# Optimization experiments

Measured on AMD Instinct MI355X. Metric: run time of the kernel, lower is better.

## Reference

```python
import math
import jax, jax.numpy as jnp
import numpy as np

B, C, NH, H, W = 8, 512, 4, 64, 64
CH = C // 8          # qkv channels = 64
HC = CH // NH        # head channels = 16


def _pos_encoding(c, h, w):
    # Faithful to torch code, including the raw memory reinterpretation of
    # pos_h (h, c) -> (1, c, h, 1) and pos_w (c//2, 2w) -> (1, c, 1, w).
    ph = jnp.arange(h, dtype=jnp.float32)[:, None]            # (h, 1)
    pw = jnp.arange(w, dtype=jnp.float32)[None, :]            # (1, w)
    div = jnp.exp(jnp.arange(0, c, 2, dtype=jnp.float32) * (-(math.log(10000.0) / c)))
    pos_h = ph * div[None, :]                                  # (h, c/2)
    pos_w = pw * div[:, None]                                  # (c/2, w)
    pos_h = jnp.concatenate([jnp.sin(pos_h), jnp.cos(pos_h)], axis=1)  # (h, c)
    pos_w = jnp.concatenate([jnp.sin(pos_w), jnp.cos(pos_w)], axis=1)  # (c/2, 2w)
    pos_h = pos_h.reshape(1, c, h, 1)   # raw view, as in torch
    pos_w = pos_w.reshape(1, c, 1, w)   # raw view, as in torch
    return pos_h + pos_w                # (1, c, h, w)


def _conv1x1(x, w, b):
    return jnp.einsum('bchw,oc->bohw', x, w) + b[None, :, None, None]


def setup_inputs() -> dict:
    key = jax.random.key(0)
    ks = jax.random.split(key, 6)
    s = 0.02
    return {
        'x':  jax.random.normal(ks[0], (B, C, H, W), dtype=jnp.float32),
        'wq': jax.random.normal(ks[1], (CH, C), dtype=jnp.float32) * s,
        'bq': jnp.zeros((CH,), dtype=jnp.float32),
        'wk': jax.random.normal(ks[2], (CH, C), dtype=jnp.float32) * s,
        'bk': jnp.zeros((CH,), dtype=jnp.float32),
        'wv': jax.random.normal(ks[3], (CH, C), dtype=jnp.float32) * s,
        'bv': jnp.zeros((CH,), dtype=jnp.float32),
        'wo': jax.random.normal(ks[4], (C, CH), dtype=jnp.float32) * s,
        'bo': jnp.zeros((C,), dtype=jnp.float32),
        'gamma': jnp.full((1,), 0.5, dtype=jnp.float32),  # nonzero to exercise whole graph
    }


def reference(x, wq, bq, wk, bk, wv, bv, wo, bo, gamma):
    b, c, h, w = x.shape
    nh, hc = NH, HC
    x = x + _pos_encoding(c, h, w)

    q = _conv1x1(x, wq, bq).reshape(b, nh, hc, h, w)
    k = _conv1x1(x, wk, bk).reshape(b, nh, hc, h, w)
    v = _conv1x1(x, wv, bv).reshape(b, nh, hc, h, w)

    # column (H) and row (W) views
    q_H = q.transpose(0, 1, 4, 2, 3).reshape(b * nh * w, hc, h).transpose(0, 2, 1)  # (bnw, h, hc)
    q_W = q.transpose(0, 1, 3, 2, 4).reshape(b * nh * h, hc, w).transpose(0, 2, 1)  # (bnh, w, hc)
    k_H = k.transpose(0, 1, 4, 2, 3).reshape(b * nh * w, hc, h)
    k_W = k.transpose(0, 1, 3, 2, 4).reshape(b * nh * h, hc, w)
    v_H = v.transpose(0, 1, 4, 2, 3).reshape(b * nh * w, hc, h)
    v_W = v.transpose(0, 1, 3, 2, 4).reshape(b * nh * h, hc, w)

    inf_mask = jnp.where(jnp.eye(h, dtype=bool), -jnp.inf, 0.0).astype(x.dtype)  # (h, h)
    energy_H = (jnp.matmul(q_H, k_H) + inf_mask[None]).reshape(b, nh, w, h, h).transpose(0, 2, 1, 3, 4)  # (b,w,nh,h,h)
    energy_W = jnp.matmul(q_W, k_W).reshape(b, nh, h, w, w).transpose(0, 2, 1, 3, 4)                     # (b,h,nh,w,w)

    conc = jax.nn.softmax(jnp.concatenate([energy_H, energy_W], axis=4), axis=4)  # (b,w,nh,h,h+w)

    att_H = conc[..., :h].transpose(0, 2, 1, 3, 4).reshape(b * nh * w, h, h)
    # NOTE: faithful to torch: (b,h,nh,w,w) is flattened in (b,h,nh) order
    att_W = conc[..., h:h + w].reshape(b * nh * h, w, w)

    out_H = jnp.matmul(v_H, att_H.transpose(0, 2, 1))
    out_H = out_H.reshape(b, nh, w, hc, h).transpose(0, 3, 4, 1, 2).reshape(b, nh * hc, h, w)
    out_W = jnp.matmul(v_W, att_W.transpose(0, 2, 1))
    out_W = out_W.reshape(b, nh, h, hc, w).transpose(0, 3, 1, 4, 2).reshape(b, nh * hc, h, w)

    out = _conv1x1(out_H + out_W, wo, bo)
    return gamma * out + x
```

## Files before the change

kernel.cpp:

```cpp
#include <hip/hip_runtime.h>
#include <math.h>


typedef unsigned int u32;
typedef unsigned short u16;
typedef __attribute__((ext_vector_type(8))) short short8;
typedef __attribute__((ext_vector_type(4))) float f32x4;

__device__ __forceinline__ u16 f2bf(float v) {
    u32 u = __float_as_uint(v);
    u32 r = (u + 0x7FFFu + ((u >> 16) & 1u)) >> 16;
    return (u16)r;
}

__device__ __forceinline__ float bf2f(u16 v) {
    return __uint_as_float(((u32)v) << 16);
}

__device__ __forceinline__ void gll16(const void* g, void* l) {
    __builtin_amdgcn_global_load_lds(
        (const __attribute__((address_space(1))) u32*)g,
        (__attribute__((address_space(3))) u32*)l, 16, 0, 0);
}

__global__ __launch_bounds__(64) void pos_kernel(float* __restrict__ PH,
                                                 float* __restrict__ PW) {
    const float r = 0.03597789207798663f;
    int c = blockIdx.x;
    int t = threadIdx.x;
    int i = c >> 3;
    int j = ((c & 7) << 6) | t;
    float ph;
    if (j < 256) ph = sinf((float)i * expf(-(float)j * r));
    else         ph = cosf((float)i * expf(-(float)(j - 256) * r));
    PH[c * 64 + t] = ph;
    int tt = c >> 1;
    float dv = expf(-(float)tt * r);
    PW[c * 64 + t] = (c & 1) ? cosf((float)t * dv) : sinf((float)t * dv);
}

__global__ __launch_bounds__(256) void wconv_kernel(
    const float* __restrict__ wq, const float* __restrict__ wk,
    const float* __restrict__ wv, const float* __restrict__ wo,
    u16* __restrict__ WT, u16* __restrict__ WOb) {
    int i = blockIdx.x * 256 + threadIdx.x;
    if (i < 98304) {
        float v;
        if (i < 32768)      v = wq[i];
        else if (i < 65536) v = wk[i - 32768];
        else                v = wv[i - 65536];
        WT[i] = f2bf(v);
    } else {
        WOb[i - 98304] = f2bf(wo[i - 98304]);
    }
}

__global__ __launch_bounds__(256) void wpos_kernel(
    const float* __restrict__ wq, const float* __restrict__ wk,
    const float* __restrict__ wv,
    const float* __restrict__ PH, const float* __restrict__ PW,
    float* __restrict__ WPH3, float* __restrict__ WPW3) {
    int gid = blockIdx.x * 256 + threadIdx.x;
    int h = gid & 63;
    int m = (gid >> 6) & 63;
    int t = gid >> 12;
    int mg = t >> 1, tbl = t & 1;
    const float* W = (mg == 0) ? wq : (mg == 1) ? wk : wv;
    const float* P = tbl ? PW : PH;
    const float* wr = W + m * 512;
    float s = 0.f;
#pragma unroll 8
    for (int c = 0; c < 512; ++c) s += wr[c] * P[c * 64 + h];
    (tbl ? WPW3 : WPH3)[(mg * 64 + m) * 64 + h] = s;
}

__global__ __launch_bounds__(256) void qkvx_kernel(
    const float* __restrict__ x, const u16* __restrict__ WT,
    const float* __restrict__ bq, const float* __restrict__ bk,
    const float* __restrict__ bv,
    const float* __restrict__ WPH3, const float* __restrict__ WPW3,
    u16* __restrict__ QHt, u16* __restrict__ QWt,
    u16* __restrict__ KHt, u16* __restrict__ KWt,
    u16* __restrict__ VHt, u16* __restrict__ Vb) {
    __shared__ u16 Wb[192 * 64];
    __shared__ u16 Bb[64 * 64];
    int L  = blockIdx.x;
    int b  = L & 7;
    int pt = L >> 3;
    int tid  = threadIdx.x;
    int w    = tid >> 6;
    int lane = tid & 63;
    int ln15 = lane & 15, quad = lane >> 4;

    f32x4 acc[12];
#pragma unroll
    for (int mf = 0; mf < 12; ++mf) acc[mf] = (f32x4){0.f, 0.f, 0.f, 0.f};

    const float* xb = x + (size_t)b * 2097152 + pt * 64;

    for (int kc = 0; kc < 512; kc += 64) {
        __syncthreads();
#pragma unroll
        for (int it = 0; it < 6; ++it) {
            int idx = tid + it * 256;
            int r = idx >> 3, s = idx & 7;
            gll16(WT + r * 512 + kc + ((s ^ (r & 7)) * 8), &Wb[idx * 8]);
        }
#pragma unroll
        for (int j = 0; j < 2; ++j) {
            int cc = w + j * 4;
            const float* xp = xb + (size_t)(kc + cc * 8) * 4096 + lane;
            float v[8];
#pragma unroll
            for (int i = 0; i < 8; ++i) v[i] = xp[(size_t)i * 4096];
            short8 pk;
#pragma unroll
            for (int i = 0; i < 8; ++i) pk[i] = (short)f2bf(v[i]);
            *(short8*)&Bb[lane * 64 + ((cc ^ (lane & 7)) * 8)] = pk;
        }
        __syncthreads();
#pragma unroll
        for (int ks = 0; ks < 2; ++ks) {
            int cs = ks * 4 + quad;
            int brow = w * 16 + ln15;
            short8 bf = *(const short8*)&Bb[brow * 64 + ((cs ^ (brow & 7)) * 8)];
#pragma unroll
            for (int mf = 0; mf < 12; ++mf) {
                int arow = mf * 16 + ln15;
                short8 af = *(const short8*)&Wb[arow * 64 + ((cs ^ (arow & 7)) * 8)];
                acc[mf] = __builtin_amdgcn_mfma_f32_16x16x32_bf16(
                    af, bf, acc[mf], 0, 0, 0);
            }
        }
    }

    int wc = w * 16 + ln15;
#pragma unroll
    for (int mf = 0; mf < 12; ++mf) {
        int mg = mf >> 2, nm = mf & 3;
        const float* bias = (mg == 0) ? bq : (mg == 1) ? bk : bv;
        float vals[4];
#pragma unroll
        for (int reg = 0; reg < 4; ++reg) {
            int m2 = nm * 16 + quad * 4 + reg;
            vals[reg] = acc[mf][reg] + bias[m2]
                      + WPH3[(mg * 64 + m2) * 64 + pt]
                      + WPW3[(mg * 64 + m2) * 64 + wc];
        }
        if (mg == 2) {
#pragma unroll
            for (int reg = 0; reg < 4; ++reg) {
                int hc = quad * 4 + reg;
                u16 bv16 = f2bf(vals[reg]);
                VHt[(((b * 4 + nm) * 64 + wc) * 16 + hc) * 64 + pt] = bv16;
                Vb[((size_t)(b * 64 + nm * 16 + hc)) * 4096 + pt * 64 + wc] = bv16;
            }
        } else {
            u16* Ht = (mg == 1) ? KHt : QHt;
            u16* Wt = (mg == 1) ? KWt : QWt;
            ushort4 pk;
            pk.x = f2bf(vals[0]);
            pk.y = f2bf(vals[1]);
            pk.z = f2bf(vals[2]);
            pk.w = f2bf(vals[3]);
            *(ushort4*)&Ht[(((b * 4 + nm) * 64 + wc) * 64 + pt) * 16 + quad * 4] = pk;
            *(ushort4*)&Wt[(((b * 4 + nm) * 64 + pt) * 64 + wc) * 16 + quad * 4] = pk;
        }
    }
}

__global__ __launch_bounds__(256, 4) void attn_kernel(
    const u16* __restrict__ QHt, const u16* __restrict__ QWt,
    const u16* __restrict__ KHt, const u16* __restrict__ KWt,
    const u16* __restrict__ VHt, const u16* __restrict__ Vb,
    u16* __restrict__ OHc, u16* __restrict__ OWc) {
    __shared__ u16 U[11008];
    u16* A_lds  = U;
    u16* B_lds  = U + 2560;
    u16* P_lds  = U;
    u16* VH_lds = U + 8704;
    u16* VW_lds = U + 9856;

    int a = blockIdx.x, n = blockIdx.y, b = blockIdx.z;
    int tid  = threadIdx.x;
    int w    = tid >> 6;
    int lane = tid & 63;
    int ln15 = lane & 15, quad = lane >> 4;
    int nv = a >> 4;
    int hv = ((a & 15) << 2) | n;

    const int cb = ((b * 4 + n) * 64 + a) << 10;
    const u16* vb = Vb + ((size_t)(b * 64 + nv * 16)) * 4096 + hv * 64;

    {
        int t = tid & 127;
        const short8 z8 = {0, 0, 0, 0, 0, 0, 0, 0};
        if (tid < 128) {
            short8 vA = *(const short8*)(QHt + cb + t * 8);
            *(short8*)&A_lds[(t >> 1) * 40 + (t & 1) * 8] = vA;
            short8 vK = *(const short8*)(KHt + cb + t * 8);
            *(short8*)&B_lds[(t >> 1) * 48 + (t & 1) * 8] = vK;
            *(short8*)&B_lds[(t >> 1) * 48 + 16 + (t & 1) * 8] = z8;
            short8 vV = *(const short8*)(VHt + cb + t * 8);
            *(short8*)&VH_lds[(t >> 3) * 72 + (t & 7) * 8] = vV;
        } else {
            short8 vA = *(const short8*)(QWt + cb + t * 8);
            *(short8*)&A_lds[(t >> 1) * 40 + 16 + (t & 1) * 8] = vA;
            short8 vK = *(const short8*)(KWt + cb + t * 8);
            *(short8*)&B_lds[(64 + (t >> 1)) * 48 + 16 + (t & 1) * 8] = vK;
            *(short8*)&B_lds[(64 + (t >> 1)) * 48 + (t & 1) * 8] = z8;
            short8 vV = *(const short8*)(vb + (t >> 3) * 4096 + (t & 7) * 8);
            *(short8*)&VW_lds[(t >> 3) * 72 + (t & 7) * 8] = vV;
        }
    }
    __syncthreads();

    const f32x4 zf = {0.f, 0.f, 0.f, 0.f};
    short8 af = *(const short8*)&A_lds[(w * 16 + ln15) * 40 + quad * 8];
    f32x4 acc[8];
#pragma unroll
    for (int nt = 0; nt < 8; ++nt) {
        short8 bf = *(const short8*)&B_lds[(nt * 16 + ln15) * 48 + quad * 8];
        acc[nt] = __builtin_amdgcn_mfma_f32_16x16x32_bf16(af, bf, zf, 0, 0, 0);
    }

#pragma unroll
    for (int nt = 0; nt < 4; ++nt)
#pragma unroll
        for (int r = 0; r < 4; ++r)
            if (nt * 16 + ln15 == w * 16 + quad * 4 + r) acc[nt][r] = -1e30f;

    float inv[4];
#pragma unroll
    for (int r = 0; r < 4; ++r) {
        float mrow = acc[0][r];
#pragma unroll
        for (int nt = 1; nt < 8; ++nt) mrow = fmaxf(mrow, acc[nt][r]);
        mrow = fmaxf(mrow, __shfl_xor(mrow, 1, 64));
        mrow = fmaxf(mrow, __shfl_xor(mrow, 2, 64));
        mrow = fmaxf(mrow, __shfl_xor(mrow, 4, 64));
        mrow = fmaxf(mrow, __shfl_xor(mrow, 8, 64));
        float s = 0.f;
#pragma unroll
        for (int nt = 0; nt < 8; ++nt) {
            float e = __expf(acc[nt][r] - mrow);
            acc[nt][r] = e;
            s += e;
        }
        s += __shfl_xor(s, 1, 64);
        s += __shfl_xor(s, 2, 64);
        s += __shfl_xor(s, 4, 64);
        s += __shfl_xor(s, 8, 64);
        inv[r] = 1.0f / s;
    }
    __syncthreads();
#pragma unroll
    for (int nt = 0; nt < 8; ++nt)
#pragma unroll
        for (int r = 0; r < 4; ++r)
            P_lds[(w * 16 + quad * 4 + r) * 136 + nt * 16 + ln15] =
                f2bf(acc[nt][r] * inv[r]);
    __syncthreads();

    int prow = (w * 16 + ln15) * 136;
    short8 a0 = *(const short8*)&P_lds[prow +       quad * 8];
    short8 a1 = *(const short8*)&P_lds[prow + 32  + quad * 8];
    short8 a2 = *(const short8*)&P_lds[prow + 64  + quad * 8];
    short8 a3 = *(const short8*)&P_lds[prow + 96  + quad * 8];
    short8 b0 = *(const short8*)&VH_lds[ln15 * 72 +      quad * 8];
    short8 b1 = *(const short8*)&VH_lds[ln15 * 72 + 32 + quad * 8];
    short8 c0 = *(const short8*)&VW_lds[ln15 * 72 +      quad * 8];
    short8 c1 = *(const short8*)&VW_lds[ln15 * 72 + 32 + quad * 8];
    f32x4 oH = __builtin_amdgcn_mfma_f32_16x16x32_bf16(a0, b0, zf, 0, 0, 0);
    oH = __builtin_amdgcn_mfma_f32_16x16x32_bf16(a1, b1, oH, 0, 0, 0);
    f32x4 oW = __builtin_amdgcn_mfma_f32_16x16x32_bf16(a2, c0, zf, 0, 0, 0);
    oW = __builtin_amdgcn_mfma_f32_16x16x32_bf16(a3, c1, oW, 0, 0, 0);

    __syncthreads();
    u16* eph = U;
    u16* epw = U + 16 * 68;
#pragma unroll
    for (int r = 0; r < 4; ++r) {
        eph[(quad * 4 + r) * 68 + ln15 * 4 + w]   = f2bf(oH[r]);
        epw[(w * 16 + quad * 4 + r) * 20 + ln15]  = f2bf(oW[r]);
    }
    __syncthreads();
    {
        int t = tid;
        ushort4 vh = *(const ushort4*)&eph[(t >> 4) * 68 + (t & 15) * 4];
        ushort4 vw = *(const ushort4*)&epw[(t >> 2) * 20 + (t & 3) * 4];
        size_t cbase = (((size_t)b * 4 + n) * 64 + a) * 1024;
        *(ushort4*)&OHc[cbase + t * 4] = vh;
        *(ushort4*)&OWc[cbase + t * 4] = vw;
    }
}

__global__ __launch_bounds__(256) void sconv_kernel(
    const u16* __restrict__ OHc, const u16* __restrict__ OWc,
    u16* __restrict__ Sb) {
    int h = blockIdx.x;
    int b = blockIdx.y;
    int t  = threadIdx.x;
    int wp = t >> 2;
    int cq = t & 3;

    const u16* ohp = OHc + ((((size_t)b * 4 + (h & 3)) * 64 + wp) * 1024
                            + (h >> 2) * 64 + cq * 16);
    short8 oh0 = *(const short8*)ohp;
    short8 oh1 = *(const short8*)(ohp + 8);

    const u16* owb = OWc + (((size_t)b * 4 + (wp & 3)) * 64) * 1024 + h * 16 + cq * 4;
    ushort4 owv[4];
#pragma unroll
    for (int nvi = 0; nvi < 4; ++nvi)
        owv[nvi] = *(const ushort4*)(owb + (size_t)((nvi << 4) | (wp >> 2)) * 1024);

    u16 res[16];
#pragma unroll
    for (int j = 0; j < 16; ++j) {
        u16 ohv = (j < 8) ? (u16)oh0[j] : (u16)oh1[j - 8];
        const ushort4& q = owv[j & 3];
        u16 owu = (j >> 2) == 0 ? q.x : (j >> 2) == 1 ? q.y : (j >> 2) == 2 ? q.z : q.w;
        res[j] = f2bf(bf2f(ohv) + bf2f(owu));
    }
    u16* dst = Sb + (((size_t)b * 4096 + h * 64 + wp) * 64 + cq * 16);
    *(short8*)dst       = *(short8*)&res[0];
    *(short8*)(dst + 8) = *(short8*)&res[8];
}

__global__ __launch_bounds__(256, 4) void finalm_kernel(
    const u16* __restrict__ Sb, const u16* __restrict__ WOb,
    const float* __restrict__ bo, const float* __restrict__ gamma,
    const float* __restrict__ x, const float* __restrict__ PH,
    const float* __restrict__ PW, float* __restrict__ out) {
    __shared__ u16 Ab[64 * 64];
    __shared__ u16 Bb[128 * 64];
    int pt = blockIdx.x;
    int mc = blockIdx.y;
    int b  = blockIdx.z;
    int tid  = threadIdx.x;
    int w    = tid >> 6;
    int lane = tid & 63;
    int ln15 = lane & 15, quad = lane >> 4;
    int p0 = pt * 128, m0 = mc * 64;

    float4 xv[4][2];
#pragma unroll
    for (int mf = 0; mf < 4; ++mf) {
        int m = m0 + mf * 16 + ln15;
#pragma unroll
        for (int pf = 0; pf < 2; ++pf) {
            int pb = p0 + w * 32 + pf * 16 + quad * 4;
            xv[mf][pf] = *(const float4*)&x[((size_t)(b * 512 + m)) * 4096 + pb];
        }
    }

    const u16* Ag = WOb + m0 * 64;
    const u16* Sg = Sb + ((size_t)b * 4096 + p0) * 64;

#pragma unroll
    for (int it = 0; it < 2; ++it) {
        int idx = tid + it * 256;
        int r = idx >> 3, s = idx & 7;
        gll16(Ag + r * 64 + ((s ^ (r & 7)) * 8), &Ab[idx * 8]);
    }
#pragma unroll
    for (int it = 0; it < 4; ++it) {
        int idx = tid + it * 256;
        int r = idx >> 3, s = idx & 7;
        gll16(Sg + r * 64 + ((s ^ (r & 7)) * 8), &Bb[idx * 8]);
    }
    __syncthreads();

    const f32x4 zf = {0.f, 0.f, 0.f, 0.f};
    f32x4 acc[4][2];
#pragma unroll
    for (int mf = 0; mf < 4; ++mf)
#pragma unroll
        for (int pf = 0; pf < 2; ++pf)
            acc[mf][pf] = zf;
#pragma unroll
    for (int ks = 0; ks < 2; ++ks) {
        int cs = ks * 4 + quad;
        short8 af[2], bf[4];
#pragma unroll
        for (int pf = 0; pf < 2; ++pf) {
            int row = w * 32 + pf * 16 + ln15;
            af[pf] = *(const short8*)&Bb[row * 64 + ((cs ^ (row & 7)) * 8)];
        }
#pragma unroll
        for (int mf = 0; mf < 4; ++mf) {
            int row = mf * 16 + ln15;
            bf[mf] = *(const short8*)&Ab[row * 64 + ((cs ^ (row & 7)) * 8)];
        }
#pragma unroll
        for (int mf = 0; mf < 4; ++mf)
#pragma unroll
            for (int pf = 0; pf < 2; ++pf)
                acc[mf][pf] = __builtin_amdgcn_mfma_f32_16x16x32_bf16(
                    af[pf], bf[mf], acc[mf][pf], 0, 0, 0);
    }

    float g = gamma[0];
    int h = pt * 2 + (w >> 1);
    int plb = (w & 1) * 32;
#pragma unroll
    for (int mf = 0; mf < 4; ++mf) {
        int m = m0 + mf * 16 + ln15;
        float bm = bo[m];
        float ph = PH[m * 64 + h];
#pragma unroll
        for (int pf = 0; pf < 2; ++pf) {
            int pb = p0 + w * 32 + pf * 16 + quad * 4;
            size_t o = ((size_t)(b * 512 + m)) * 4096 + pb;
            float4 pwv = *(const float4*)&PW[m * 64 + plb + pf * 16 + quad * 4];
            float4 res;
            res.x = g * (acc[mf][pf][0] + bm) + xv[mf][pf].x + ph + pwv.x;
            res.y = g * (acc[mf][pf][1] + bm) + xv[mf][pf].y + ph + pwv.y;
            res.z = g * (acc[mf][pf][2] + bm) + xv[mf][pf].z + ph + pwv.z;
            res.w = g * (acc[mf][pf][3] + bm) + xv[mf][pf].w + ph + pwv.w;
            *(float4*)&out[o] = res;
        }
    }
}

extern "C" void kernel_launch(void* const* d_in, const int* in_sizes, int n_in,
                              void* d_out, int out_size, void* d_ws, size_t ws_size,
                              hipStream_t stream) {
    const float* x     = (const float*)d_in[0];
    const float* wq    = (const float*)d_in[1];
    const float* bq    = (const float*)d_in[2];
    const float* wk    = (const float*)d_in[3];
    const float* bk    = (const float*)d_in[4];
    const float* wv    = (const float*)d_in[5];
    const float* bv    = (const float*)d_in[6];
    const float* wo    = (const float*)d_in[7];
    const float* bo    = (const float*)d_in[8];
    const float* gamma = (const float*)d_in[9];
    float* out = (float*)d_out;
    float* ws  = (float*)d_ws;

    float* PH   = ws;
    float* PW   = PH + 32768;
    float* WPH3 = PW + 32768;
    float* WPW3 = WPH3 + 12288;
    u16*   WT   = (u16*)(WPW3 + 12288);
    u16*   WOb  = WT + 98304;
    u16*   QHt  = WOb + 32768;
    u16*   QWt  = QHt + 2097152;
    u16*   KHt  = QWt + 2097152;
    u16*   KWt  = KHt + 2097152;
    u16*   VHt  = KWt + 2097152;
    u16*   Vb   = VHt + 2097152;
    u16*   OHc  = Vb  + 2097152;
    u16*   OWc  = OHc + 2097152;
    u16*   Sbb  = OWc + 2097152;

    pos_kernel<<<dim3(512), dim3(64), 0, stream>>>(PH, PW);
    wconv_kernel<<<dim3(512), dim3(256), 0, stream>>>(wq, wk, wv, wo, WT, WOb);
    wpos_kernel<<<dim3(96), dim3(256), 0, stream>>>(wq, wk, wv, PH, PW, WPH3, WPW3);
    qkvx_kernel<<<dim3(512), dim3(256), 0, stream>>>(
        x, WT, bq, bk, bv, WPH3, WPW3, QHt, QWt, KHt, KWt, VHt, Vb);
    attn_kernel<<<dim3(64, 4, 8), dim3(256), 0, stream>>>(
        QHt, QWt, KHt, KWt, VHt, Vb, OHc, OWc);
    sconv_kernel<<<dim3(64, 8), dim3(256), 0, stream>>>(OHc, OWc, Sbb);
    finalm_kernel<<<dim3(32, 8, 8), dim3(256), 0, stream>>>(
        Sbb, WOb, bo, gamma, x, PH, PW, out);
}
```

Measured before the change: 207.3 us.

## Double-buffer QKV projection LDS tiles and retile warps as 2x2 MFMA grid

The QKV projection kernel now double-buffers its weight and x tiles in LDS. The next K-chunk's global loads are issued before the MFMAs on the current chunk, and the bf16 conversion and store happen after them, so memory latency overlaps with compute and there is one barrier per step instead of two. Warps are also remapped from 12 M-fragments by 1 N-fragment to 6 by 2, which lowers the LDS A-fragment reads per MFMA. The cost is double the LDS footprint (about 57KB) and extra registers for the prefetched x values, which may reduce occupancy.

```diff
diff --git a/kernel.cpp b/kernel.cpp
--- a/kernel.cpp
+++ b/kernel.cpp
@@ -82,8 +82,8 @@
     u16* __restrict__ QHt, u16* __restrict__ QWt,
     u16* __restrict__ KHt, u16* __restrict__ KWt,
     u16* __restrict__ VHt, u16* __restrict__ Vb) {
-    __shared__ u16 Wb[192 * 64];
-    __shared__ u16 Bb[64 * 64];
+    __shared__ u16 Wb[2][192 * 64];
+    __shared__ u16 Bb[2][64 * 64];
     int L  = blockIdx.x;
     int b  = L & 7;
     int pt = L >> 3;
@@ -91,80 +91,130 @@
     int w    = tid >> 6;
     int lane = tid & 63;
     int ln15 = lane & 15, quad = lane >> 4;
-
-    f32x4 acc[12];
-#pragma unroll
-    for (int mf = 0; mf < 12; ++mf) acc[mf] = (f32x4){0.f, 0.f, 0.f, 0.f};
+    int wm = w >> 1;
+    int wp = w & 1;
+
+    f32x4 acc[6][2];
+#pragma unroll
+    for (int i = 0; i < 6; ++i)
+#pragma unroll
+        for (int pf = 0; pf < 2; ++pf)
+            acc[i][pf] = (f32x4){0.f, 0.f, 0.f, 0.f};
 
     const float* xb = x + (size_t)b * 2097152 + pt * 64;
 
-    for (int kc = 0; kc < 512; kc += 64) {
-        __syncthreads();
-#pragma unroll
-        for (int it = 0; it < 6; ++it) {
-            int idx = tid + it * 256;
-            int r = idx >> 3, s = idx & 7;
-            gll16(WT + r * 512 + kc + ((s ^ (r & 7)) * 8), &Wb[idx * 8]);
-        }
-#pragma unroll
-        for (int j = 0; j < 2; ++j) {
-            int cc = w + j * 4;
-            const float* xp = xb + (size_t)(kc + cc * 8) * 4096 + lane;
-            float v[8];
-#pragma unroll
-            for (int i = 0; i < 8; ++i) v[i] = xp[(size_t)i * 4096];
-            short8 pk;
-#pragma unroll
-            for (int i = 0; i < 8; ++i) pk[i] = (short)f2bf(v[i]);
-            *(short8*)&Bb[lane * 64 + ((cc ^ (lane & 7)) * 8)] = pk;
-        }
-        __syncthreads();
+    float v[2][8];
+#pragma unroll
+    for (int it = 0; it < 6; ++it) {
+        int idx = tid + it * 256;
+        int r = idx >> 3, s = idx & 7;
+        gll16(WT + r * 512 + ((s ^ (r & 7)) * 8), &Wb[0][idx * 8]);
+    }
+#pragma unroll
+    for (int j = 0; j < 2; ++j) {
+        int cc = w + j * 4;
+        const float* xp = xb + (size_t)(cc * 8) * 4096 + lane;
+#pragma unroll
+        for (int i = 0; i < 8; ++i) v[j][i] = xp[(size_t)i * 4096];
+    }
+#pragma unroll
+    for (int j = 0; j < 2; ++j) {
+        int cc = w + j * 4;
+        short8 pk;
+#pragma unroll
+        for (int i = 0; i < 8; ++i) pk[i] = (short)f2bf(v[j][i]);
+        *(short8*)&Bb[0][lane * 64 + ((cc ^ (lane & 7)) * 8)] = pk;
+    }
+    __syncthreads();
+
+    int cur = 0;
+    for (int step = 0; step < 8; ++step) {
+        int nxt = cur ^ 1;
+        bool more = (step < 7);
+        if (more) {
+            int kc = (step + 1) * 64;
+#pragma unroll
+            for (int it = 0; it < 6; ++it) {
+                int idx = tid + it * 256;
+                int r = idx >> 3, s = idx & 7;
+                gll16(WT + r * 512 + kc + ((s ^ (r & 7)) * 8), &Wb[nxt][idx * 8]);
+            }
+#pragma unroll
+            for (int j = 0; j < 2; ++j) {
+                int cc = w + j * 4;
+                const float* xp = xb + (size_t)(kc + cc * 8) * 4096 + lane;
+#pragma unroll
+                for (int i = 0; i < 8; ++i) v[j][i] = xp[(size_t)i * 4096];
+            }
+        }
 #pragma unroll
         for (int ks = 0; ks < 2; ++ks) {
             int cs = ks * 4 + quad;
-            int brow = w * 16 + ln15;
-            short8 bf = *(const short8*)&Bb[brow * 64 + ((cs ^ (brow & 7)) * 8)];
-#pragma unroll
-            for (int mf = 0; mf < 12; ++mf) {
-                int arow = mf * 16 + ln15;
-                short8 af = *(const short8*)&Wb[arow * 64 + ((cs ^ (arow & 7)) * 8)];
-                acc[mf] = __builtin_amdgcn_mfma_f32_16x16x32_bf16(
-                    af, bf, acc[mf], 0, 0, 0);
-            }
-        }
-    }
-
-    int wc = w * 16 + ln15;
-#pragma unroll
-    for (int mf = 0; mf < 12; ++mf) {
+            short8 bf[2];
+#pragma unroll
+            for (int pf = 0; pf < 2; ++pf) {
+                int brow = wp * 32 + pf * 16 + ln15;
+                bf[pf] = *(const short8*)&Bb[cur][brow * 64 + ((cs ^ (brow & 7)) * 8)];
+            }
+#pragma unroll
+            for (int i = 0; i < 6; ++i) {
+                int arow = (wm * 6 + i) * 16 + ln15;
+                short8 af = *(const short8*)&Wb[cur][arow * 64 + ((cs ^ (arow & 7)) * 8)];
+#pragma unroll
+                for (int pf = 0; pf < 2; ++pf)
+                    acc[i][pf] = __builtin_amdgcn_mfma_f32_16x16x32_bf16(
+                        af, bf[pf], acc[i][pf], 0, 0, 0);
+            }
+        }
+        if (more) {
+#pragma unroll
+            for (int j = 0; j < 2; ++j) {
+                int cc = w + j * 4;
+                short8 pk;
+#pragma unroll
+                for (int i = 0; i < 8; ++i) pk[i] = (short)f2bf(v[j][i]);
+                *(short8*)&Bb[nxt][lane * 64 + ((cc ^ (lane & 7)) * 8)] = pk;
+            }
+            __syncthreads();
+        }
+        cur = nxt;
+    }
+
+#pragma unroll
+    for (int i = 0; i < 6; ++i) {
+        int mf = wm * 6 + i;
         int mg = mf >> 2, nm = mf & 3;
         const float* bias = (mg == 0) ? bq : (mg == 1) ? bk : bv;
-        float vals[4];
-#pragma unroll
-        for (int reg = 0; reg < 4; ++reg) {
-            int m2 = nm * 16 + quad * 4 + reg;
-            vals[reg] = acc[mf][reg] + bias[m2]
-                      + WPH3[(mg * 64 + m2) * 64 + pt]
-                      + WPW3[(mg * 64 + m2) * 64 + wc];
-        }
-        if (mg == 2) {
+#pragma unroll
+        for (int pf = 0; pf < 2; ++pf) {
+            int wc = wp * 32 + pf * 16 + ln15;
+            float vals[4];
 #pragma unroll
             for (int reg = 0; reg < 4; ++reg) {
-                int hc = quad * 4 + reg;
-                u16 bv16 = f2bf(vals[reg]);
-                VHt[(((b * 4 + nm) * 64 + wc) * 16 + hc) * 64 + pt] = bv16;
-                Vb[((size_t)(b * 64 + nm * 16 + hc)) * 4096 + pt * 64 + wc] = bv16;
-            }
-        } else {
-            u16* Ht = (mg == 1) ? KHt : QHt;
-            u16* Wt = (mg == 1) ? KWt : QWt;
-            ushort4 pk;
-            pk.x = f2bf(vals[0]);
-            pk.y = f2bf(vals[1]);
-            pk.z = f2bf(vals[2]);
-            pk.w = f2bf(vals[3]);
-            *(ushort4*)&Ht[(((b * 4 + nm) * 64 + wc) * 64 + pt) * 16 + quad * 4] = pk;
-            *(ushort4*)&Wt[(((b * 4 + nm) * 64 + pt) * 64 + wc) * 16 + quad * 4] = pk;
+                int m2 = nm * 16 + quad * 4 + reg;
+                vals[reg] = acc[i][pf][reg] + bias[m2]
+                          + WPH3[(mg * 64 + m2) * 64 + pt]
+                          + WPW3[(mg * 64 + m2) * 64 + wc];
+            }
+            if (mg == 2) {
+#pragma unroll
+                for (int reg = 0; reg < 4; ++reg) {
+                    int hc = quad * 4 + reg;
+                    u16 bv16 = f2bf(vals[reg]);
+                    VHt[(((b * 4 + nm) * 64 + wc) * 16 + hc) * 64 + pt] = bv16;
+                    Vb[((size_t)(b * 64 + nm * 16 + hc)) * 4096 + pt * 64 + wc] = bv16;
+                }
+            } else {
+                u16* Ht = (mg == 1) ? KHt : QHt;
+                u16* Wt = (mg == 1) ? KWt : QWt;
+                ushort4 pk;
+                pk.x = f2bf(vals[0]);
+                pk.y = f2bf(vals[1]);
+                pk.z = f2bf(vals[2]);
+                pk.w = f2bf(vals[3]);
+                *(ushort4*)&Ht[(((b * 4 + nm) * 64 + wc) * 64 + pt) * 16 + quad * 4] = pk;
+                *(ushort4*)&Wt[(((b * 4 + nm) * 64 + pt) * 64 + wc) * 16 + quad * 4] = pk;
+            }
         }
     }
 }
```

New measurement: 205.3 us. About the same (-1.0%).

## Double-buffer QKV projection LDS stages and retile warps to 6x2 MFMA blocks

Applied to the files above, without the earlier changes.

The QKV projection GEMM now uses double-buffered LDS for the weight and x tiles. The next chunk's weight async-copy and the x global loads (two chunks ahead, held in registers) are issued before the current chunk's MFMAs, with explicit waitcnt and barrier scheduling. Warps are retiled from each owning 12 M-fragments by 1 N-fragment to 6 by 2, so each A fragment read from LDS feeds two MFMAs. This aims to hide global-load latency and cut LDS traffic, at the cost of twice the LDS footprint, extra registers for the prefetched x values, and fragile hand-written vmcnt counts.

```diff
diff --git a/kernel.cpp b/kernel.cpp
--- a/kernel.cpp
+++ b/kernel.cpp
@@ -82,8 +82,8 @@
     u16* __restrict__ QHt, u16* __restrict__ QWt,
     u16* __restrict__ KHt, u16* __restrict__ KWt,
     u16* __restrict__ VHt, u16* __restrict__ Vb) {
-    __shared__ u16 Wb[192 * 64];
-    __shared__ u16 Bb[64 * 64];
+    __shared__ u16 Wb[2][192 * 64];
+    __shared__ u16 Bb[2][64 * 64];
     int L  = blockIdx.x;
     int b  = L & 7;
     int pt = L >> 3;
@@ -91,80 +91,151 @@
     int w    = tid >> 6;
     int lane = tid & 63;
     int ln15 = lane & 15, quad = lane >> 4;
-
-    f32x4 acc[12];
-#pragma unroll
-    for (int mf = 0; mf < 12; ++mf) acc[mf] = (f32x4){0.f, 0.f, 0.f, 0.f};
+    int wm = w >> 1;
+    int wp = w & 1;
+
+    f32x4 acc[6][2];
+#pragma unroll
+    for (int i = 0; i < 6; ++i)
+#pragma unroll
+        for (int pf = 0; pf < 2; ++pf)
+            acc[i][pf] = (f32x4){0.f, 0.f, 0.f, 0.f};
 
     const float* xb = x + (size_t)b * 2097152 + pt * 64;
 
-    for (int kc = 0; kc < 512; kc += 64) {
-        __syncthreads();
-#pragma unroll
-        for (int it = 0; it < 6; ++it) {
-            int idx = tid + it * 256;
-            int r = idx >> 3, s = idx & 7;
-            gll16(WT + r * 512 + kc + ((s ^ (r & 7)) * 8), &Wb[idx * 8]);
-        }
-#pragma unroll
-        for (int j = 0; j < 2; ++j) {
-            int cc = w + j * 4;
-            const float* xp = xb + (size_t)(kc + cc * 8) * 4096 + lane;
-            float v[8];
-#pragma unroll
-            for (int i = 0; i < 8; ++i) v[i] = xp[(size_t)i * 4096];
-            short8 pk;
-#pragma unroll
-            for (int i = 0; i < 8; ++i) pk[i] = (short)f2bf(v[i]);
-            *(short8*)&Bb[lane * 64 + ((cc ^ (lane & 7)) * 8)] = pk;
-        }
-        __syncthreads();
-#pragma unroll
-        for (int ks = 0; ks < 2; ++ks) {
-            int cs = ks * 4 + quad;
-            int brow = w * 16 + ln15;
-            short8 bf = *(const short8*)&Bb[brow * 64 + ((cs ^ (brow & 7)) * 8)];
-#pragma unroll
-            for (int mf = 0; mf < 12; ++mf) {
-                int arow = mf * 16 + ln15;
-                short8 af = *(const short8*)&Wb[arow * 64 + ((cs ^ (arow & 7)) * 8)];
-                acc[mf] = __builtin_amdgcn_mfma_f32_16x16x32_bf16(
-                    af, bf, acc[mf], 0, 0, 0);
-            }
-        }
-    }
-
-    int wc = w * 16 + ln15;
-#pragma unroll
-    for (int mf = 0; mf < 12; ++mf) {
+    float va[2][8], vb[2][8];
+
+#define WSTAGE(BUF, KC)                                                     \
+    {                                                                       \
+        _Pragma("unroll")                                                   \
+        for (int it = 0; it < 6; ++it) {                                    \
+            int idx = tid + it * 256;                                       \
+            int r = idx >> 3, s = idx & 7;                                  \
+            gll16(WT + r * 512 + (KC) + ((s ^ (r & 7)) * 8),                \
+                  &Wb[BUF][idx * 8]);                                       \
+        }                                                                   \
+    }
+
+#define XLOAD(DST, KC)                                                      \
+    {                                                                       \
+        _Pragma("unroll")                                                   \
+        for (int j = 0; j < 2; ++j) {                                       \
+            int cc = w + j * 4;                                             \
+            const float* xp = xb + (size_t)((KC) + cc * 8) * 4096 + lane;   \
+            _Pragma("unroll")                                               \
+            for (int i = 0; i < 8; ++i) DST[j][i] = xp[(size_t)i * 4096];   \
+        }                                                                   \
+    }
+
+#define XPACK(SRC, BUF)                                                     \
+    {                                                                       \
+        _Pragma("unroll")                                                   \
+        for (int j = 0; j < 2; ++j) {                                       \
+            int cc = w + j * 4;                                             \
+            short8 pk;                                                      \
+            _Pragma("unroll")                                               \
+            for (int i = 0; i < 8; ++i) pk[i] = (short)f2bf(SRC[j][i]);     \
+            *(short8*)&Bb[BUF][lane * 64 + ((cc ^ (lane & 7)) * 8)] = pk;   \
+        }                                                                   \
+    }
+
+#define MFMA_STEP(BUF)                                                      \
+    {                                                                       \
+        _Pragma("unroll")                                                   \
+        for (int ks = 0; ks < 2; ++ks) {                                    \
+            int cs = ks * 4 + quad;                                         \
+            short8 bf[2];                                                   \
+            _Pragma("unroll")                                               \
+            for (int pf = 0; pf < 2; ++pf) {                                \
+                int brow = wp * 32 + pf * 16 + ln15;                        \
+                bf[pf] = *(const short8*)&Bb[BUF][brow * 64 +               \
+                             ((cs ^ (brow & 7)) * 8)];                      \
+            }                                                               \
+            _Pragma("unroll")                                               \
+            for (int i = 0; i < 6; ++i) {                                   \
+                int arow = (wm * 6 + i) * 16 + ln15;                        \
+                short8 af = *(const short8*)&Wb[BUF][arow * 64 +            \
+                                ((cs ^ (arow & 7)) * 8)];                   \
+                _Pragma("unroll")                                           \
+                for (int pf = 0; pf < 2; ++pf)                              \
+                    acc[i][pf] = __builtin_amdgcn_mfma_f32_16x16x32_bf16(   \
+                        af, bf[pf], acc[i][pf], 0, 0, 0);                   \
+            }                                                               \
+        }                                                                   \
+    }
+
+    WSTAGE(0, 0);
+    XLOAD(va, 0);
+    XLOAD(vb, 64);
+    __builtin_amdgcn_sched_barrier(0);
+    XPACK(va, 0);
+    asm volatile("s_waitcnt vmcnt(16)" ::: "memory");
+    asm volatile("s_waitcnt lgkmcnt(0)" ::: "memory");
+    __builtin_amdgcn_sched_barrier(0);
+    __builtin_amdgcn_s_barrier();
+    __builtin_amdgcn_sched_barrier(0);
+
+#pragma unroll
+    for (int step = 0; step < 7; ++step) {
+        const int cur = step & 1, nxt = cur ^ 1;
+        WSTAGE(nxt, (step + 1) * 64);
+        if (step < 6) {
+            if ((step & 1) == 0) { XLOAD(va, (step + 2) * 64); }
+            else                 { XLOAD(vb, (step + 2) * 64); }
+        }
+        __builtin_amdgcn_sched_barrier(0);
+        MFMA_STEP(cur);
+        if ((step & 1) == 0) { XPACK(vb, nxt); }
+        else                 { XPACK(va, nxt); }
+        if (step < 6) asm volatile("s_waitcnt vmcnt(16)" ::: "memory");
+        else          asm volatile("s_waitcnt vmcnt(0)"  ::: "memory");
+        asm volatile("s_waitcnt lgkmcnt(0)" ::: "memory");
+        __builtin_amdgcn_sched_barrier(0);
+        __builtin_amdgcn_s_barrier();
+        __builtin_amdgcn_sched_barrier(0);
+    }
+    MFMA_STEP(1);
+
+#undef WSTAGE
+#undef XLOAD
+#undef XPACK
+#undef MFMA_STEP
+
+#pragma unroll
+    for (int i = 0; i < 6; ++i) {
+        int mf = wm * 6 + i;
         int mg = mf >> 2, nm = mf & 3;
         const float* bias = (mg == 0) ? bq : (mg == 1) ? bk : bv;
-        float vals[4];
-#pragma unroll
-        for (int reg = 0; reg < 4; ++reg) {
-            int m2 = nm * 16 + quad * 4 + reg;
-            vals[reg] = acc[mf][reg] + bias[m2]
-                      + WPH3[(mg * 64 + m2) * 64 + pt]
-                      + WPW3[(mg * 64 + m2) * 64 + wc];
-        }
-        if (mg == 2) {
+#pragma unroll
+        for (int pf = 0; pf < 2; ++pf) {
+            int wc = wp * 32 + pf * 16 + ln15;
+            float vals[4];
 #pragma unroll
             for (int reg = 0; reg < 4; ++reg) {
-                int hc = quad * 4 + reg;
-                u16 bv16 = f2bf(vals[reg]);
-                VHt[(((b * 4 + nm) * 64 + wc) * 16 + hc) * 64 + pt] = bv16;
-                Vb[((size_t)(b * 64 + nm * 16 + hc)) * 4096 + pt * 64 + wc] = bv16;
+                int m2 = nm * 16 + quad * 4 + reg;
+                vals[reg] = acc[i][pf][reg] + bias[m2]
+                          + WPH3[(mg * 64 + m2) * 64 + pt]
+                          + WPW3[(mg * 64 + m2) * 64 + wc];
             }
-        } else {
-            u16* Ht = (mg == 1) ? KHt : QHt;
-            u16* Wt = (mg == 1) ? KWt : QWt;
-            ushort4 pk;
-            pk.x = f2bf(vals[0]);
-            pk.y = f2bf(vals[1]);
-            pk.z = f2bf(vals[2]);
-            pk.w = f2bf(vals[3]);
-            *(ushort4*)&Ht[(((b * 4 + nm) * 64 + wc) * 64 + pt) * 16 + quad * 4] = pk;
-            *(ushort4*)&Wt[(((b * 4 + nm) * 64 + pt) * 64 + wc) * 16 + quad * 4] = pk;
+            if (mg == 2) {
+#pragma unroll
+                for (int reg = 0; reg < 4; ++reg) {
+                    int hc = quad * 4 + reg;
+                    u16 bv16 = f2bf(vals[reg]);
+                    VHt[(((b * 4 + nm) * 64 + wc) * 16 + hc) * 64 + pt] = bv16;
+                    Vb[((size_t)(b * 64 + nm * 16 + hc)) * 4096 + pt * 64 + wc] = bv16;
+                }
+            } else {
+                u16* Ht = (mg == 1) ? KHt : QHt;
+                u16* Wt = (mg == 1) ? KWt : QWt;
+                ushort4 pk;
+                pk.x = f2bf(vals[0]);
+                pk.y = f2bf(vals[1]);
+                pk.z = f2bf(vals[2]);
+                pk.w = f2bf(vals[3]);
+                *(ushort4*)&Ht[(((b * 4 + nm) * 64 + wc) * 64 + pt) * 16 + quad * 4] = pk;
+                *(ushort4*)&Wt[(((b * 4 + nm) * 64 + pt) * 64 + wc) * 16 + quad * 4] = pk;
+            }
         }
     }
 }
```

Measured after the change: 205.4 us. About the same (-0.9%).

## Store Q/K/V once in a single layout and gather transposed views in attention

Applied to the files above, without the earlier changes.

The QKV projection kernel previously wrote six bf16 tensors (H- and W-oriented copies of Q, K and V). It now writes one channel-last layout per tensor, cutting its global write traffic roughly in half. The attention kernel reads the H view with strided gathers and transposes V into LDS with scalar stores. The projection kernel's warp tiling also changes to a 2x2 split (6 M-fragments by 2 N-fragments per wave) so each A fragment feeds two MFMAs, and the grid order of attn/sconv is swapped so batch varies fastest, which may help L2 locality. The cost is less-coalesced 16-byte loads and scalar LDS transposes in the attention prologue.

```diff
diff --git a/kernel.cpp b/kernel.cpp
--- a/kernel.cpp
+++ b/kernel.cpp
@@ -79,9 +79,7 @@
     const float* __restrict__ bq, const float* __restrict__ bk,
     const float* __restrict__ bv,
     const float* __restrict__ WPH3, const float* __restrict__ WPW3,
-    u16* __restrict__ QHt, u16* __restrict__ QWt,
-    u16* __restrict__ KHt, u16* __restrict__ KWt,
-    u16* __restrict__ VHt, u16* __restrict__ Vb) {
+    u16* __restrict__ Qc, u16* __restrict__ Kc, u16* __restrict__ Vc) {
     __shared__ u16 Wb[192 * 64];
     __shared__ u16 Bb[64 * 64];
     int L  = blockIdx.x;
@@ -91,10 +89,15 @@
     int w    = tid >> 6;
     int lane = tid & 63;
     int ln15 = lane & 15, quad = lane >> 4;
-
-    f32x4 acc[12];
-#pragma unroll
-    for (int mf = 0; mf < 12; ++mf) acc[mf] = (f32x4){0.f, 0.f, 0.f, 0.f};
+    int wm = w >> 1;
+    int wp = w & 1;
+
+    f32x4 acc[6][2];
+#pragma unroll
+    for (int i = 0; i < 6; ++i)
+#pragma unroll
+        for (int pf = 0; pf < 2; ++pf)
+            acc[i][pf] = (f32x4){0.f, 0.f, 0.f, 0.f};
 
     const float* xb = x + (size_t)b * 2097152 + pt * 64;
 
@@ -122,57 +125,55 @@
 #pragma unroll
         for (int ks = 0; ks < 2; ++ks) {
             int cs = ks * 4 + quad;
-            int brow = w * 16 + ln15;
-            short8 bf = *(const short8*)&Bb[brow * 64 + ((cs ^ (brow & 7)) * 8)];
-#pragma unroll
-            for (int mf = 0; mf < 12; ++mf) {
-                int arow = mf * 16 + ln15;
+            short8 bf[2];
+#pragma unroll
+            for (int pf = 0; pf < 2; ++pf) {
+                int brow = wp * 32 + pf * 16 + ln15;
+                bf[pf] = *(const short8*)&Bb[brow * 64 + ((cs ^ (brow & 7)) * 8)];
+            }
+#pragma unroll
+            for (int i = 0; i < 6; ++i) {
+                int arow = (wm * 6 + i) * 16 + ln15;
                 short8 af = *(const short8*)&Wb[arow * 64 + ((cs ^ (arow & 7)) * 8)];
-                acc[mf] = __builtin_amdgcn_mfma_f32_16x16x32_bf16(
-                    af, bf, acc[mf], 0, 0, 0);
+#pragma unroll
+                for (int pf = 0; pf < 2; ++pf)
+                    acc[i][pf] = __builtin_amdgcn_mfma_f32_16x16x32_bf16(
+                        af, bf[pf], acc[i][pf], 0, 0, 0);
             }
         }
     }
 
-    int wc = w * 16 + ln15;
-#pragma unroll
-    for (int mf = 0; mf < 12; ++mf) {
+#pragma unroll
+    for (int i = 0; i < 6; ++i) {
+        int mf = wm * 6 + i;
         int mg = mf >> 2, nm = mf & 3;
         const float* bias = (mg == 0) ? bq : (mg == 1) ? bk : bv;
-        float vals[4];
-#pragma unroll
-        for (int reg = 0; reg < 4; ++reg) {
-            int m2 = nm * 16 + quad * 4 + reg;
-            vals[reg] = acc[mf][reg] + bias[m2]
-                      + WPH3[(mg * 64 + m2) * 64 + pt]
-                      + WPW3[(mg * 64 + m2) * 64 + wc];
-        }
-        if (mg == 2) {
+        u16* T = (mg == 0) ? Qc : (mg == 1) ? Kc : Vc;
+#pragma unroll
+        for (int pf = 0; pf < 2; ++pf) {
+            int wc = wp * 32 + pf * 16 + ln15;
+            float vals[4];
 #pragma unroll
             for (int reg = 0; reg < 4; ++reg) {
-                int hc = quad * 4 + reg;
-                u16 bv16 = f2bf(vals[reg]);
-                VHt[(((b * 4 + nm) * 64 + wc) * 16 + hc) * 64 + pt] = bv16;
-                Vb[((size_t)(b * 64 + nm * 16 + hc)) * 4096 + pt * 64 + wc] = bv16;
+                int m2 = nm * 16 + quad * 4 + reg;
+                vals[reg] = acc[i][pf][reg] + bias[m2]
+                          + WPH3[(mg * 64 + m2) * 64 + pt]
+                          + WPW3[(mg * 64 + m2) * 64 + wc];
             }
-        } else {
-            u16* Ht = (mg == 1) ? KHt : QHt;
-            u16* Wt = (mg == 1) ? KWt : QWt;
             ushort4 pk;
             pk.x = f2bf(vals[0]);
             pk.y = f2bf(vals[1]);
             pk.z = f2bf(vals[2]);
             pk.w = f2bf(vals[3]);
-            *(ushort4*)&Ht[(((b * 4 + nm) * 64 + wc) * 64 + pt) * 16 + quad * 4] = pk;
-            *(ushort4*)&Wt[(((b * 4 + nm) * 64 + pt) * 64 + wc) * 16 + quad * 4] = pk;
+            *(ushort4*)&T[(((size_t)(b * 4 + nm) * 64 + pt) * 64 + wc) * 16
+                          + quad * 4] = pk;
         }
     }
 }
 
 __global__ __launch_bounds__(256, 4) void attn_kernel(
-    const u16* __restrict__ QHt, const u16* __restrict__ QWt,
-    const u16* __restrict__ KHt, const u16* __restrict__ KWt,
-    const u16* __restrict__ VHt, const u16* __restrict__ Vb,
+    const u16* __restrict__ Qc, const u16* __restrict__ Kc,
+    const u16* __restrict__ Vc,
     u16* __restrict__ OHc, u16* __restrict__ OWc) {
     __shared__ u16 U[11008];
     u16* A_lds  = U;
@@ -181,7 +182,7 @@
     u16* VH_lds = U + 8704;
     u16* VW_lds = U + 9856;
 
-    int a = blockIdx.x, n = blockIdx.y, b = blockIdx.z;
+    int b = blockIdx.x, n = blockIdx.y, a = blockIdx.z;
     int tid  = threadIdx.x;
     int w    = tid >> 6;
     int lane = tid & 63;
@@ -189,28 +190,34 @@
     int nv = a >> 4;
     int hv = ((a & 15) << 2) | n;
 
-    const int cb = ((b * 4 + n) * 64 + a) << 10;
-    const u16* vb = Vb + ((size_t)(b * 64 + nv * 16)) * 4096 + hv * 64;
+    const size_t cb = (((size_t)b * 4 + n) * 64 + a) * 1024;
 
     {
         int t = tid & 127;
         const short8 z8 = {0, 0, 0, 0, 0, 0, 0, 0};
         if (tid < 128) {
-            short8 vA = *(const short8*)(QHt + cb + t * 8);
-            *(short8*)&A_lds[(t >> 1) * 40 + (t & 1) * 8] = vA;
-            short8 vK = *(const short8*)(KHt + cb + t * 8);
-            *(short8*)&B_lds[(t >> 1) * 48 + (t & 1) * 8] = vK;
-            *(short8*)&B_lds[(t >> 1) * 48 + 16 + (t & 1) * 8] = z8;
-            short8 vV = *(const short8*)(VHt + cb + t * 8);
-            *(short8*)&VH_lds[(t >> 3) * 72 + (t & 7) * 8] = vV;
+            int h = t >> 1, half = t & 1;
+            size_t hb = (((size_t)b * 4 + n) * 64 + h) * 1024 + a * 16 + half * 8;
+            short8 vA = *(const short8*)(Qc + hb);
+            *(short8*)&A_lds[h * 40 + half * 8] = vA;
+            short8 vK = *(const short8*)(Kc + hb);
+            *(short8*)&B_lds[h * 48 + half * 8] = vK;
+            *(short8*)&B_lds[h * 48 + 16 + half * 8] = z8;
+            short8 vV = *(const short8*)(Vc + hb);
+#pragma unroll
+            for (int j = 0; j < 8; ++j)
+                VH_lds[(half * 8 + j) * 72 + h] = (u16)vV[j];
         } else {
-            short8 vA = *(const short8*)(QWt + cb + t * 8);
+            short8 vA = *(const short8*)(Qc + cb + t * 8);
             *(short8*)&A_lds[(t >> 1) * 40 + 16 + (t & 1) * 8] = vA;
-            short8 vK = *(const short8*)(KWt + cb + t * 8);
+            short8 vK = *(const short8*)(Kc + cb + t * 8);
             *(short8*)&B_lds[(64 + (t >> 1)) * 48 + 16 + (t & 1) * 8] = vK;
             *(short8*)&B_lds[(64 + (t >> 1)) * 48 + (t & 1) * 8] = z8;
-            short8 vV = *(const short8*)(vb + (t >> 3) * 4096 + (t & 7) * 8);
-            *(short8*)&VW_lds[(t >> 3) * 72 + (t & 7) * 8] = vV;
+            size_t wb2 = (((size_t)b * 4 + nv) * 64 + hv) * 1024 + t * 8;
+            short8 vV = *(const short8*)(Vc + wb2);
+#pragma unroll
+            for (int j = 0; j < 8; ++j)
+                VW_lds[((t & 1) * 8 + j) * 72 + (t >> 1)] = (u16)vV[j];
         }
     }
     __syncthreads();
@@ -298,8 +305,8 @@
 __global__ __launch_bounds__(256) void sconv_kernel(
     const u16* __restrict__ OHc, const u16* __restrict__ OWc,
     u16* __restrict__ Sb) {
-    int h = blockIdx.x;
-    int b = blockIdx.y;
+    int b = blockIdx.x;
+    int h = blockIdx.y;
     int t  = threadIdx.x;
     int wp = t >> 2;
     int cq = t & 3;
@@ -446,13 +453,10 @@
     float* WPW3 = WPH3 + 12288;
     u16*   WT   = (u16*)(WPW3 + 12288);
     u16*   WOb  = WT + 98304;
-    u16*   QHt  = WOb + 32768;
-    u16*   QWt  = QHt + 2097152;
-    u16*   KHt  = QWt + 2097152;
-    u16*   KWt  = KHt + 2097152;
-    u16*   VHt  = KWt + 2097152;
-    u16*   Vb   = VHt + 2097152;
-    u16*   OHc  = Vb  + 2097152;
+    u16*   Qc   = WOb + 32768;
+    u16*   Kc   = Qc + 2097152;
+    u16*   Vc   = Kc + 2097152;
+    u16*   OHc  = Vc + 2097152;
     u16*   OWc  = OHc + 2097152;
     u16*   Sbb  = OWc + 2097152;
 
@@ -460,10 +464,10 @@
     wconv_kernel<<<dim3(512), dim3(256), 0, stream>>>(wq, wk, wv, wo, WT, WOb);
     wpos_kernel<<<dim3(96), dim3(256), 0, stream>>>(wq, wk, wv, PH, PW, WPH3, WPW3);
     qkvx_kernel<<<dim3(512), dim3(256), 0, stream>>>(
-        x, WT, bq, bk, bv, WPH3, WPW3, QHt, QWt, KHt, KWt, VHt, Vb);
-    attn_kernel<<<dim3(64, 4, 8), dim3(256), 0, stream>>>(
-        QHt, QWt, KHt, KWt, VHt, Vb, OHc, OWc);
-    sconv_kernel<<<dim3(64, 8), dim3(256), 0, stream>>>(OHc, OWc, Sbb);
+        x, WT, bq, bk, bv, WPH3, WPW3, Qc, Kc, Vc);
+    attn_kernel<<<dim3(8, 4, 64), dim3(256), 0, stream>>>(
+        Qc, Kc, Vc, OHc, OWc);
+    sconv_kernel<<<dim3(8, 64), dim3(256), 0, stream>>>(OHc, OWc, Sbb);
     finalm_kernel<<<dim3(32, 8, 8), dim3(256), 0, stream>>>(
         Sbb, WOb, bo, gamma, x, PH, PW, out);
 }
```

Result: faster. 197.5 us (-4.7%).
